# Kernel optimization log

Hardware: AMD Instinct MI355X
Metric: run time of the kernel (lower is better)

The kernel has to match this reference:

```python
import jax, jax.numpy as jnp
import numpy as np

EPS = 1e-13  # threshold used by K.greater(x, 1e-13) in the original
STATE = 90   # fixed DP window length


def setup_inputs() -> dict:
    key = jax.random.key(0)
    k1, k2 = jax.random.split(key)
    B, L, F = 128, 8192, 9
    # 9 transcription-factor concentration tracks, strictly positive
    tf_conc = jax.random.uniform(k1, (B, L, F), dtype=jnp.float32)
    # single cooperativity weight, RandomUniform(0, 500) with NonNeg constraint
    kernel = jax.random.uniform(k2, (1,), dtype=jnp.float32) * 500.0
    return {"tf_conc": tf_conc, "kernel": kernel}


def _kenneth_single(conc, kernel):
    """conc: (L, 9) = [bcd, cad, dst, dic, hb, kr, kni, gt, tll]. Returns (9, L)."""
    dtype = conc.dtype
    # data rows per timestep: [bcd, bcd, cad, dst, dic, hb, kr, kni, gt, tll]
    data = jnp.concatenate([conc[:, :1], conc], axis=1)  # (L, 10)
    k = kernel[0]

    def step(carry, x):
        Zs, bcds = carry                      # each (90,)
        nc = x[1:]                            # (9,) non-cooperative weights
        # cooperative term: windowed dot of shifted bcd history and Z history
        c = x[0] * k * jnp.sum(bcds[15:75] * Zs[29:89])
        # NOTE: original code overwrites znow, dropping c from the recursion
        znow = jnp.sum(nc) + Zs[0]
        Zs_new = jnp.concatenate([znow[None], Zs[:-1]])
        bcds_new = jnp.concatenate([x[:1], bcds[:-1]])
        return (Zs_new, bcds_new), jnp.concatenate([c[None], nc])  # out (10,)

    init = (jnp.ones(STATE, dtype), jnp.zeros(STATE, dtype))
    (Zs_f, _), Z53 = jax.lax.scan(step, init, data)           # 5'->3' pass
    (_, _), Z35r = jax.lax.scan(step, init, data[::-1])       # 3'->5' pass
    Z35 = Z35r[::-1]                                          # reversed back
    Z1 = Zs_f[0]                                              # partition function Z[0][0]

    def adj(v):
        # v + 1 - (v > eps): replaces (near-)zero concentrations by 1 for safe division
        return v + 1.0 - (v > EPS).astype(dtype)

    f_bcd = (Z53[:, 0] * Z35[:, 1] + Z53[:, 1] * Z35[:, 0]
             + Z35[:, 1] * Z53[:, 1]) / adj(conc[:, 0]) / Z1
    fs = [f_bcd] + [(Z35[:, j] * Z53[:, j]) / adj(conc[:, j - 1]) / Z1
                    for j in range(2, 10)]
    return jnp.clip(jnp.stack(fs, axis=0), 0.0, 0.9999)  # (9, L)


def reference(tf_conc, kernel):
    # tf_conc: (B, L, 9) -> fractional occupancies (B, 9, L)
    return jax.vmap(lambda c: _kenneth_single(c, kernel))(tf_conc)
```

## Files before the change

kernel.cpp:

```cpp
#include <hip/hip_runtime.h>

#define LSEQ 8192
#define NF 9
#define CT 8
#define TSZ 1024
#define NT 256
#define IT 4
#define NW 4
#define EOFF 96
#define EB (EOFF + TSZ + 88)
#define PQB (TSZ + 76)
#define POISON 0xAAAAAAAAAAAAAAAAULL

__device__ __forceinline__ float f4c(const float4& v, int c) {
    return c == 0 ? v.x : c == 1 ? v.y : c == 2 ? v.z : v.w;
}

__global__ __launch_bounds__(NT, 4) void kenneth_fused(const float* __restrict__ conc,
                                                       const float* __restrict__ kern,
                                                       unsigned long long* __restrict__ vals,
                                                       float* __restrict__ out) {
    __shared__ __align__(16) float E[EB];
    __shared__ __align__(16) float Pfa[PQB];
    __shared__ __align__(16) float Qba[PQB];
    __shared__ float Ah[76], Af[75];
    __shared__ double scr[NW];
    __shared__ double sBuf[CT];

    const int bc = blockIdx.x;
    const int b = bc / CT, c = bc % CT;
    const int t0g = c * TSZ;
    const int tid = threadIdx.x, lane = tid & 63, wid = tid >> 6;
    const int x0 = tid * IT;

    const float* __restrict__ cp = conc + (size_t)b * LSEQ * NF;
    float* __restrict__ op = out + (size_t)b * NF * LSEQ;
    const float4* __restrict__ p4 = (const float4*)(cp + (size_t)(t0g + x0) * NF);

    float4 q[9];
    #pragma unroll
    for (int m = 0; m < 9; ++m) q[m] = p4[m];

    const float kf = kern[0];

    float hs = 0.f, hcol0 = 0.f;
    if (tid < 184) {
        int t = (tid < 96) ? (t0g - 96 + tid) : (t0g + TSZ + (tid - 96));
        if (t >= 0 && t < LSEQ) {
            const float* r = cp + (size_t)t * NF;
            float s0 = r[0];
            hcol0 = s0;
            float ss = s0;
            #pragma unroll
            for (int m = 1; m < 9; ++m) ss += r[m];
            hs = ss;
        }
    }

    float av[IT], Sv[IT];
    #pragma unroll
    for (int i = 0; i < IT; ++i) {
        float s = 0.f;
        #pragma unroll
        for (int cc2 = 0; cc2 < 9; ++cc2) {
            int idx = 9 * i + cc2;
            float val = f4c(q[idx >> 2], idx & 3);
            if (cc2 == 0) av[i] = val;
            s += val;
        }
        Sv[i] = s;
    }

    if (tid < 96) E[tid] = hs;
    else if (tid < 184) E[EOFF + TSZ + (tid - 96)] = hs;
    if (tid >= 20 && tid < 96) Ah[tid - 20] = hcol0;
    if (tid >= 96 && tid < 171) Af[tid - 96] = hcol0;

    double incl[IT];
    double run = 0.0;
    #pragma unroll
    for (int i = 0; i < IT; ++i) { run += (double)Sv[i]; incl[i] = run; }
    double v = run;
    #pragma unroll
    for (int off = 1; off < 64; off <<= 1) {
        double n = __shfl_up(v, (unsigned)off, 64);
        if (lane >= off) v += n;
    }
    if (lane == 63) scr[wid] = v;
    __syncthreads();
    double wOff = 0.0, bT = 0.0;
    #pragma unroll
    for (int w = 0; w < NW; ++w) {
        double t2 = scr[w];
        if (w < wid) wOff += t2;
        bT += t2;
    }
    if (tid == 0) {
        atomicExch(&vals[bc], (unsigned long long)__double_as_longlong(bT));
    }
    double excl = wOff + (v - run);
    {
        float4 w = make_float4((float)(excl + incl[0]), (float)(excl + incl[1]),
                               (float)(excl + incl[2]), (float)(excl + incl[3]));
        *(float4*)&E[EOFF + x0] = w;
    }

    if (wid == 0) {
        float r0 = 0.f, r1 = 0.f;
        if (lane < 48) { r0 = E[2 * lane]; r1 = E[2 * lane + 1]; }
        double ps = (double)r0 + (double)r1;
        double inc = ps;
        #pragma unroll
        for (int off = 1; off < 64; off <<= 1) {
            double n = __shfl_up(inc, (unsigned)off, 64);
            if (lane >= off) inc += n;
        }
        double tot96 = __shfl(inc, 63, 64);
        if (lane < 48) {
            E[2 * lane]     = (float)((inc - ps) + (double)r0 - tot96);
            E[2 * lane + 1] = (float)(inc - tot96);
        }
    } else if (wid == 1) {
        const int base = EOFF + TSZ;
        float r0 = 0.f, r1 = 0.f;
        if (lane < 44) { r0 = E[base + 2 * lane]; r1 = E[base + 2 * lane + 1]; }
        double ps = (double)r0 + (double)r1;
        double inc = ps;
        #pragma unroll
        for (int off = 1; off < 64; off <<= 1) {
            double n = __shfl_up(inc, (unsigned)off, 64);
            if (lane >= off) inc += n;
        }
        if (lane < 44) {
            E[base + 2 * lane]     = (float)(bT + (inc - ps) + (double)r0);
            E[base + 2 * lane + 1] = (float)(bT + inc);
        }
    }

    if (tid < CT) {
        unsigned long long uv;
        while ((uv = atomicAdd(&vals[b * CT + tid], 0ULL)) == POISON) {
            __builtin_amdgcn_s_sleep(2);
        }
        sBuf[tid] = __longlong_as_double((long long)uv);
    }
    __syncthreads();

    double offS = 0.0, totS = 0.0;
    #pragma unroll
    for (int cc = 0; cc < CT; ++cc) {
        double vv = sBuf[cc];
        if (cc < c) offS += vv;
        totS += vv;
    }
    const float invZ1 = (float)(1.0 / (1.0 + totS));

    #pragma unroll
    for (int r = 1; r < 9; ++r) {
        float4 w;
        float* wp = (float*)&w;
        #pragma unroll
        for (int i = 0; i < IT; ++i) {
            int idx = 9 * i + r;
            float vv = f4c(q[idx >> 2], idx & 3);
            float sel = (vv > 1e-13f) ? vv
                        : vv * (vv * __builtin_amdgcn_rcpf(vv + 1.0f));
            float f = sel * invZ1;
            wp[i] = fminf(fmaxf(f, 0.0f), 0.9999f);
        }
        *(float4*)(op + (size_t)r * LSEQ + t0g + x0) = w;
    }

    const double zoff = 1.0 + offS;
    const double woff = 1.0 + totS - offS;
    {
        float pv[IT], qv[IT];
        #pragma unroll
        for (int i = 0; i < IT; ++i) {
            int x = x0 + i;
            pv[i] = av[i] * (float)(zoff + (double)E[EOFF + x - 14]);
            qv[i] = av[i] * (float)(woff - (double)E[EOFF + x + 13]);
        }
        #pragma unroll
        for (int i = 0; i < IT; ++i) Pfa[x0 + 75 + i] = pv[i];
        if (x0 >= 16) {
            *(float4*)&Qba[x0 - 16] = make_float4(qv[0], qv[1], qv[2], qv[3]);
        } else {
            #pragma unroll
            for (int i = 0; i < IT; ++i) if (x0 + i >= 16) Qba[x0 + i - 16] = qv[i];
        }
    }
    if (tid < 75) {
        Pfa[tid] = Ah[tid + 1] * (float)(zoff + (double)E[tid + 7]);
        Qba[TSZ - 16 + tid] = Af[tid] * (float)(woff - (double)E[EOFF + TSZ + tid + 13]);
    }
    __syncthreads();

    float cfw[IT], cbw[IT];
    {
        const float4* Pf4 = (const float4*)&Pfa[x0];
        float4 pa = Pf4[0], pb = Pf4[15];
        float4 s4 = pa;
        #pragma unroll
        for (int m = 1; m < 15; ++m) { float4 t = Pf4[m]; s4.x += t.x; s4.y += t.y; s4.z += t.z; s4.w += t.w; }
        cfw[0] = (s4.x + s4.y) + (s4.z + s4.w);
        cfw[1] = cfw[0] - pa.x + pb.x;
        cfw[2] = cfw[1] - pa.y + pb.y;
        cfw[3] = cfw[2] - pa.z + pb.z;
    }
    {
        const float4* Qb4 = (const float4*)&Qba[x0];
        float4 pa = Qb4[0], pb = Qb4[15];
        float4 s4 = pa;
        #pragma unroll
        for (int m = 1; m < 15; ++m) { float4 t = Qb4[m]; s4.x += t.x; s4.y += t.y; s4.z += t.z; s4.w += t.w; }
        cbw[0] = (s4.x + s4.y) + (s4.z + s4.w);
        cbw[1] = cbw[0] - pa.x + pb.x;
        cbw[2] = cbw[1] - pa.y + pb.y;
        cbw[3] = cbw[2] - pa.z + pb.z;
    }

    float fo[IT];
    #pragma unroll
    for (int i = 0; i < IT; ++i) {
        float a = av[i];
        float cf = kf * a * cfw[i];
        float cb = kf * a * cbw[i];
        float t1 = cf + cb + a;
        float sel0 = (a > 1e-13f) ? 1.0f : a * __builtin_amdgcn_rcpf(a + 1.0f);
        float f = t1 * sel0 * invZ1;
        fo[i] = fminf(fmaxf(f, 0.0f), 0.9999f);
    }
    *(float4*)(op + t0g + x0) = make_float4(fo[0], fo[1], fo[2], fo[3]);
}

extern "C" void kernel_launch(void* const* d_in, const int* in_sizes, int n_in,
                              void* d_out, int out_size, void* d_ws, size_t ws_size,
                              hipStream_t stream) {
    const float* conc = (const float*)d_in[0];
    const float* kern = (const float*)d_in[1];
    float* out = (float*)d_out;
    unsigned long long* vals = (unsigned long long*)d_ws;
    int B = in_sizes[0] / (LSEQ * NF);
    hipLaunchKernelGGL(kenneth_fused, dim3(B * CT), dim3(NT), 0, stream,
                       conc, kern, vals, out);
}
```

Before: 89.62 us.

## Halve tile size to double block count and precompute selection terms before spin-wait

Splits each sequence into 16 chunks of 512 timesteps with 128-thread blocks instead of 8 chunks of 1024, doubling the grid so more blocks are resident and fewer threads sit idle during the cross-block wait. Halo loading is reorganised so the backward and forward halos are fetched by the same low-numbered threads, since there are now fewer threads per block. The per-factor near-zero selection is computed before the inter-block spin-wait rather than after it, moving arithmetic off the critical path at the cost of 32 more live registers. Smaller tiles raise the halo overhead relative to useful work and add more global atomics and spin-polling blocks per sequence.

```diff
diff --git a/kernel.cpp b/kernel.cpp
--- a/kernel.cpp
+++ b/kernel.cpp
@@ -2,11 +2,11 @@
 
 #define LSEQ 8192
 #define NF 9
-#define CT 8
-#define TSZ 1024
-#define NT 256
+#define CT 16
+#define TSZ 512
+#define NT 128
 #define IT 4
-#define NW 4
+#define NW 2
 #define EOFF 96
 #define EB (EOFF + TSZ + 88)
 #define PQB (TSZ + 76)
@@ -28,7 +28,7 @@
     __shared__ double sBuf[CT];
 
     const int bc = blockIdx.x;
-    const int b = bc / CT, c = bc % CT;
+    const int b = bc >> 4, c = bc & 15;
     const int t0g = c * TSZ;
     const int tid = threadIdx.x, lane = tid & 63, wid = tid >> 6;
     const int x0 = tid * IT;
@@ -43,21 +43,32 @@
 
     const float kf = kern[0];
 
-    float hs = 0.f, hcol0 = 0.f;
-    if (tid < 184) {
-        int t = (tid < 96) ? (t0g - 96 + tid) : (t0g + TSZ + (tid - 96));
-        if (t >= 0 && t < LSEQ) {
+    float hsB = 0.f, hc0B = 0.f, hsF = 0.f, hc0F = 0.f;
+    if (tid < 96) {
+        int t = t0g - 96 + tid;
+        if (t >= 0) {
             const float* r = cp + (size_t)t * NF;
-            float s0 = r[0];
-            hcol0 = s0;
+            float s0 = r[0]; hc0B = s0;
             float ss = s0;
             #pragma unroll
             for (int m = 1; m < 9; ++m) ss += r[m];
-            hs = ss;
+            hsB = ss;
+        }
+    }
+    if (tid < 88) {
+        int t = t0g + TSZ + tid;
+        if (t < LSEQ) {
+            const float* r = cp + (size_t)t * NF;
+            float s0 = r[0]; hc0F = s0;
+            float ss = s0;
+            #pragma unroll
+            for (int m = 1; m < 9; ++m) ss += r[m];
+            hsF = ss;
         }
     }
 
     float av[IT], Sv[IT];
+    float selv[8][IT];
     #pragma unroll
     for (int i = 0; i < IT; ++i) {
         float s = 0.f;
@@ -66,15 +77,20 @@
             int idx = 9 * i + cc2;
             float val = f4c(q[idx >> 2], idx & 3);
             if (cc2 == 0) av[i] = val;
+            else {
+                float sel = (val > 1e-13f) ? val
+                            : val * (val * __builtin_amdgcn_rcpf(val + 1.0f));
+                selv[cc2 - 1][i] = sel;
+            }
             s += val;
         }
         Sv[i] = s;
     }
 
-    if (tid < 96) E[tid] = hs;
-    else if (tid < 184) E[EOFF + TSZ + (tid - 96)] = hs;
-    if (tid >= 20 && tid < 96) Ah[tid - 20] = hcol0;
-    if (tid >= 96 && tid < 171) Af[tid - 96] = hcol0;
+    if (tid < 96) E[tid] = hsB;
+    if (tid < 88) E[EOFF + TSZ + tid] = hsF;
+    if (tid >= 20 && tid < 96) Ah[tid - 20] = hc0B;
+    if (tid < 75) Af[tid] = hc0F;
 
     double incl[IT];
     double run = 0.0;
@@ -120,7 +136,7 @@
             E[2 * lane]     = (float)((inc - ps) + (double)r0 - tot96);
             E[2 * lane + 1] = (float)(inc - tot96);
         }
-    } else if (wid == 1) {
+    } else {
         const int base = EOFF + TSZ;
         float r0 = 0.f, r1 = 0.f;
         if (lane < 44) { r0 = E[base + 2 * lane]; r1 = E[base + 2 * lane + 1]; }
@@ -161,11 +177,7 @@
         float* wp = (float*)&w;
         #pragma unroll
         for (int i = 0; i < IT; ++i) {
-            int idx = 9 * i + r;
-            float vv = f4c(q[idx >> 2], idx & 3);
-            float sel = (vv > 1e-13f) ? vv
-                        : vv * (vv * __builtin_amdgcn_rcpf(vv + 1.0f));
-            float f = sel * invZ1;
+            float f = selv[r - 1][i] * invZ1;
             wp[i] = fminf(fmaxf(f, 0.0f), 0.9999f);
         }
         *(float4*)(op + (size_t)r * LSEQ + t0g + x0) = w;
```

New measurement: 91.85 us. 1.02x slower.
